# Optimization experiments

Hardware: AMD Instinct MI355X
Metric: run time of the kernel (lower is better)

Reference implementation:

```python
import jax, jax.numpy as jnp
import numpy as np

IN_DIM = 2048


def setup_inputs() -> dict:
    key = jax.random.key(0)
    ks = jax.random.split(key, 7)
    s = 1.0 / np.sqrt(IN_DIM)
    x = jax.random.normal(ks[0], (8, 256, IN_DIM), dtype=jnp.float32)
    Wq = jax.random.uniform(ks[1], (IN_DIM, IN_DIM), jnp.float32, -s, s)
    bq = jax.random.uniform(ks[2], (IN_DIM,), jnp.float32, -s, s)
    Wk = jax.random.uniform(ks[3], (IN_DIM, IN_DIM), jnp.float32, -s, s)
    bk = jax.random.uniform(ks[4], (IN_DIM,), jnp.float32, -s, s)
    Wv = jax.random.uniform(ks[5], (IN_DIM, IN_DIM), jnp.float32, -s, s)
    bv = jax.random.uniform(ks[6], (IN_DIM,), jnp.float32, -s, s)
    return {"x": x, "Wq": Wq, "bq": bq, "Wk": Wk, "bk": bk, "Wv": Wv, "bv": bv}


def reference(x, Wq, bq, Wk, bk, Wv, bv):
    # x: [B, C, L]; Linear acts on last (L) axis; torch Linear: y = x @ W^T + b
    scale = 1.0 / jnp.sqrt(jnp.asarray(x.shape[-1], x.dtype))
    q = jnp.einsum('bcl,ml->bcm', x, Wq) + bq
    k = jnp.einsum('bcl,ml->bcm', x, Wk) + bk
    v = jnp.einsum('bcl,ml->bcm', x, Wv) + bv
    # attn[b,l,m] = sum_c q[b,c,l] * k[b,c,m]
    attn = jnp.einsum('bcl,bcm->blm', q, k) * scale  # [B, L, L]
    attn = jax.nn.softmax(attn, axis=-1)
    # out[b,c,l] = sum_m v[b,c,m] * attn[b,l,m]
    out = jnp.einsum('bcm,blm->bcl', v, attn)  # [B, C, L]
    return out
```

## Files before the change

### kernel.cpp

```cpp
#include <hip/hip_runtime.h>
#include <hip/hip_bf16.h>
#include <cstdint>
#include <cstddef>


typedef __bf16 bf16_t;
typedef _Float16 fp16_t;
typedef __bf16 bf16x8 __attribute__((ext_vector_type(8)));
typedef __bf16 bf16x4 __attribute__((ext_vector_type(4)));
typedef float floatx4 __attribute__((ext_vector_type(4)));

#define GLD_LDS16(gptr, lptr)                                                  \
  __builtin_amdgcn_global_load_lds(                                            \
      (const __attribute__((address_space(1))) void*)(gptr),                   \
      (__attribute__((address_space(3))) void*)(lptr), 16, 0, 0)

#define BARRAW()                                                               \
  do {                                                                         \
    __builtin_amdgcn_sched_barrier(0);                                         \
    asm volatile("" ::: "memory");                                             \
    __builtin_amdgcn_s_barrier();                                              \
    __builtin_amdgcn_sched_barrier(0);                                         \
  } while (0)

__global__ __launch_bounds__(256) void cvt4_f32_bf16(
    const float* __restrict__ s0, const float* __restrict__ s1,
    const float* __restrict__ s2, const float* __restrict__ s3,
    bf16_t* __restrict__ d0, bf16_t* __restrict__ d1,
    bf16_t* __restrict__ d2, bf16_t* __restrict__ d3) {
  const float* s;
  bf16_t* d;
  switch (blockIdx.y) {
    case 0: s = s0; d = d0; break;
    case 1: s = s1; d = d1; break;
    case 2: s = s2; d = d2; break;
    default: s = s3; d = d3; break;
  }
  const int i = (blockIdx.x * 256 + threadIdx.x) * 4;
  const float4 v = *reinterpret_cast<const float4*>(s + i);
  bf16x4 o;
  o[0] = (bf16_t)v.x; o[1] = (bf16_t)v.y; o[2] = (bf16_t)v.z; o[3] = (bf16_t)v.w;
  *reinterpret_cast<bf16x4*>(d + i) = o;
}

__global__ __launch_bounds__(512, 2) void gemm_qkv8(
    const bf16_t* __restrict__ xb, const bf16_t* __restrict__ Wp,
    bf16_t* __restrict__ tT, bf16_t* __restrict__ vb,
    const float* __restrict__ bq, const float* __restrict__ bk,
    const float* __restrict__ bv) {
  __shared__ __align__(16) bf16_t As[2 * 16384];
  __shared__ __align__(16) bf16_t Bs[2 * 16384];

  constexpr long M4 = 4l * 1024 * 1024;
  const int tid = threadIdx.x, lane = tid & 63, w = tid >> 6;
  const int i15 = lane & 15, g4 = lane >> 4;
  const int wm = w >> 2, wn = w & 3;

  const int o = blockIdx.x;
  const int swz = (o & 7) * 24 + (o >> 3);
  const int mx = swz & 7, nx = swz >> 3;
  const int brow = mx * 256, bcol = nx * 256;

  const int srow = tid >> 2, sslot = tid & 3;
  const bf16_t* Ag = xb + (size_t)(brow + srow) * 2048 + sslot * 8;
  const bf16_t* Bg = Wp + (size_t)(bcol + srow) * 2048 + sslot * 8;

  auto stage_ht = [&](int h) {
    const int tile = h >> 2, buf = tile & 1, part = h & 3;
    const int kk = part >> 1;
    const bool isA = part & 1;
    const bf16_t* g = (isA ? Ag : Bg) + tile * 64 + kk * 32;
    bf16_t* l = (isA ? As : Bs) + buf * 16384 + kk * 8192 + w * 512;
    GLD_LDS16(g, l);
    GLD_LDS16(g + (size_t)128 * 2048, l + 4096);
  };

  floatx4 acc[8][4];
#pragma unroll
  for (int m = 0; m < 8; m++)
#pragma unroll
    for (int n = 0; n < 4; n++) acc[m][n] = (floatx4)0.f;

  bf16x8 Ar[4], Br[4];

#define LDA(buf, kk, mh)                                                       \
  {                                                                            \
    const bf16_t* ab = As + (buf) * 16384 + (kk) * 8192 +                      \
                       (wm * 128 + (mh) * 64 + i15) * 32 + g4 * 8;             \
    Ar[0] = *(const bf16x8*)&ab[0 * 512];                                      \
    Ar[1] = *(const bf16x8*)&ab[1 * 512];                                      \
    Ar[2] = *(const bf16x8*)&ab[2 * 512];                                      \
    Ar[3] = *(const bf16x8*)&ab[3 * 512];                                      \
  }
#define LDB(buf, kk)                                                           \
  {                                                                            \
    const bf16_t* bb = Bs + (buf) * 16384 + (kk) * 8192 +                      \
                       (wn * 64 + i15) * 32 + g4 * 8;                          \
    Br[0] = *(const bf16x8*)&bb[0 * 512];                                      \
    Br[1] = *(const bf16x8*)&bb[1 * 512];                                      \
    Br[2] = *(const bf16x8*)&bb[2 * 512];                                      \
    Br[3] = *(const bf16x8*)&bb[3 * 512];                                      \
  }
#define MMA(mh)                                                                \
  {                                                                            \
    __builtin_amdgcn_s_setprio(1);                                             \
    _Pragma("unroll") for (int mf = 0; mf < 4; mf++)                           \
        _Pragma("unroll") for (int nf = 0; nf < 4; nf++)                       \
        acc[(mh) * 4 + mf][nf] = __builtin_amdgcn_mfma_f32_16x16x32_bf16(      \
            Ar[mf], Br[nf], acc[(mh) * 4 + mf][nf], 0, 0, 0);                  \
    __builtin_amdgcn_s_setprio(0);                                             \
  }

  for (int h = 0; h < 7; ++h) stage_ht(h);
  asm volatile("s_waitcnt vmcnt(6)" ::: "memory");
  BARRAW();

  for (int j = 0; j < 16; ++j) {
    const int hb = 8 * j + 6;
    LDB(0, 0); LDA(0, 0, 0);
    stage_ht(hb + 1); BARRAW(); MMA(0); BARRAW();
    LDA(0, 0, 1);
    if (hb + 2 < 128) stage_ht(hb + 2); BARRAW(); MMA(1); BARRAW();
    LDB(0, 1); LDA(0, 1, 0);
    if (hb + 3 < 128) stage_ht(hb + 3); BARRAW(); MMA(0);
    BARRAW();
    LDA(0, 1, 1);
    if (hb + 4 < 128) stage_ht(hb + 4); BARRAW(); MMA(1);
    __builtin_amdgcn_sched_barrier(0);
    if (j == 15)
      asm volatile("s_waitcnt vmcnt(0)" ::: "memory");
    else
      asm volatile("s_waitcnt vmcnt(6)" ::: "memory");
    BARRAW();
    LDB(1, 0); LDA(1, 0, 0);
    if (hb + 5 < 128) stage_ht(hb + 5); BARRAW(); MMA(0); BARRAW();
    LDA(1, 0, 1);
    if (hb + 6 < 128) stage_ht(hb + 6); BARRAW(); MMA(1); BARRAW();
    LDB(1, 1); LDA(1, 1, 0);
    if (hb + 7 < 128) stage_ht(hb + 7); BARRAW(); MMA(0); BARRAW();
    LDA(1, 1, 1);
    if (hb + 8 < 128) stage_ht(hb + 8); BARRAW(); MMA(1);
    __builtin_amdgcn_sched_barrier(0);
    if (j < 15) asm volatile("s_waitcnt vmcnt(6)" ::: "memory");
    BARRAW();
  }
#undef LDA
#undef LDB
#undef MMA

#pragma unroll
  for (int nf = 0; nf < 4; nf++) {
    const int gj = bcol + wn * 64 + nf * 16 + i15;
    const int z = gj >> 11, jj = gj & 2047;
    const float* bp = (z == 0) ? bq : (z == 1) ? bk : bv;
    const float badd = bp[jj];
#pragma unroll
    for (int mf = 0; mf < 8; mf++) {
      const int gi = brow + wm * 128 + mf * 16 + g4 * 4;
      if (z < 2) {
        bf16x4 ov;
#pragma unroll
        for (int r = 0; r < 4; r++) ov[r] = (bf16_t)(acc[mf][nf][r] + badd);
        *(bf16x4*)&tT[(size_t)z * M4 + (size_t)jj * 2048 + gi] = ov;
      } else {
#pragma unroll
        for (int r = 0; r < 4; r++)
          vb[(size_t)(gi + r) * 2048 + jj] = (bf16_t)(acc[mf][nf][r] + badd);
      }
    }
  }
}

__global__ __launch_bounds__(256, 2) void flash3(
    const bf16_t* __restrict__ qT, const bf16_t* __restrict__ kT,
    const bf16_t* __restrict__ v, fp16_t* __restrict__ po,
    float* __restrict__ pl) {
  __shared__ __align__(16) bf16_t Ks[8192];
  __shared__ __align__(16) bf16_t Vs[8192];
  __shared__ __align__(16) bf16_t Ps[4 * 1280];

  const int tid = threadIdx.x, lane = tid & 63, w = tid >> 6;
  const int idx = blockIdx.x;
  const int b = idx & 7, sg = (idx >> 3) & 3, qt = idx >> 5;
  const int l0 = qt * 128;
  const int key0 = sg * 512;
  const int i15 = lane & 15, g4 = lane >> 4;

  const bf16_t* Qg = qT + (size_t)(l0 + w * 32) * 2048 + b * 256;
  const bf16_t* Kg = kT + (size_t)key0 * 2048 + b * 256;
  const bf16_t* Vg = v + (size_t)b * 256 * 2048 + key0;

  bf16x8 af0[8], af1[8];
#pragma unroll
  for (int ks = 0; ks < 8; ks++) {
    af0[ks] = *(const bf16x8*)&Qg[(size_t)i15 * 2048 + ks * 32 + g4 * 8];
    af1[ks] = *(const bf16x8*)&Qg[(size_t)(16 + i15) * 2048 + ks * 32 + g4 * 8];
  }

  const int srow = lane >> 2;
  const int sslot = (lane & 3) ^ ((lane >> 3) & 3);
  auto stageK = [&](const bf16_t* g) {
#pragma unroll
    for (int j = 0; j < 4; j++) {
      const int ch = w * 4 + j, ks = ch >> 1, mseg = ch & 1;
      GLD_LDS16(g + (size_t)(mseg * 16 + srow) * 2048 + ks * 32 + sslot * 8,
                Ks + ch * 512);
    }
  };
  auto stageV = [&](const bf16_t* g) {
#pragma unroll
    for (int j = 0; j < 4; j++) {
      const int ch = w * 4 + j;
      GLD_LDS16(g + (size_t)(ch * 16 + srow) * 2048 + sslot * 8, Vs + ch * 512);
    }
  };

  floatx4 acc_o0[16], acc_o1[16];
#pragma unroll
  for (int cf = 0; cf < 16; cf++) {
    acc_o0[cf] = (floatx4)0.f;
    acc_o1[cf] = (floatx4)0.f;
  }
  floatx4 acc_l0 = (floatx4)0.f, acc_l1 = (floatx4)0.f;

  bf16x8 vones;
#pragma unroll
  for (int j = 0; j < 8; j++) vones[j] = (bf16_t)1.0f;

  const float SC = 0.031880107f;
  const int slotr = g4 ^ ((i15 >> 1) & 3);

  stageK(Kg);
  stageV(Vg);
  __syncthreads();

  for (int t = 0; t < 16; t++) {
    floatx4 s00 = (floatx4)0.f, s01 = (floatx4)0.f;
    floatx4 s10 = (floatx4)0.f, s11 = (floatx4)0.f;
#pragma unroll
    for (int ks = 0; ks < 8; ks++) {
      const bf16x8 b0 = *(const bf16x8*)&Ks[ks * 1024 + i15 * 32 + slotr * 8];
      const bf16x8 b1 =
          *(const bf16x8*)&Ks[ks * 1024 + (16 + i15) * 32 + slotr * 8];
      s00 = __builtin_amdgcn_mfma_f32_16x16x32_bf16(af0[ks], b0, s00, 0, 0, 0);
      s01 = __builtin_amdgcn_mfma_f32_16x16x32_bf16(af0[ks], b1, s01, 0, 0, 0);
      s10 = __builtin_amdgcn_mfma_f32_16x16x32_bf16(af1[ks], b0, s10, 0, 0, 0);
      s11 = __builtin_amdgcn_mfma_f32_16x16x32_bf16(af1[ks], b1, s11, 0, 0, 0);
    }
    __syncthreads();
    if (t < 15) stageK(Kg + (size_t)(t + 1) * 32 * 2048);

    bf16_t* Pw = Ps + w * 1280;
#pragma unroll
    for (int r = 0; r < 4; r++) {
      Pw[(g4 * 4 + r) * 40 + i15] = (bf16_t)exp2f(s00[r] * SC);
      Pw[(g4 * 4 + r) * 40 + 16 + i15] = (bf16_t)exp2f(s01[r] * SC);
      Pw[(16 + g4 * 4 + r) * 40 + i15] = (bf16_t)exp2f(s10[r] * SC);
      Pw[(16 + g4 * 4 + r) * 40 + 16 + i15] = (bf16_t)exp2f(s11[r] * SC);
    }
    const bf16x8 pa0 = *(const bf16x8*)&Pw[i15 * 40 + g4 * 8];
    const bf16x8 pa1 = *(const bf16x8*)&Pw[(16 + i15) * 40 + g4 * 8];
    acc_l0 = __builtin_amdgcn_mfma_f32_16x16x32_bf16(pa0, vones, acc_l0, 0, 0, 0);
    acc_l1 = __builtin_amdgcn_mfma_f32_16x16x32_bf16(pa1, vones, acc_l1, 0, 0, 0);
#pragma unroll
    for (int cf = 0; cf < 16; cf++) {
      const bf16x8 bv = *(const bf16x8*)&Vs[(cf * 16 + i15) * 32 + slotr * 8];
      acc_o0[cf] = __builtin_amdgcn_mfma_f32_16x16x32_bf16(pa0, bv, acc_o0[cf], 0, 0, 0);
      acc_o1[cf] = __builtin_amdgcn_mfma_f32_16x16x32_bf16(pa1, bv, acc_o1[cf], 0, 0, 0);
    }
    __syncthreads();
    if (t < 15) stageV(Vg + (t + 1) * 32);
  }

  fp16_t* pob = po + ((size_t)(b * 4 + sg) * 2048 + l0 + w * 32) * 256;
#pragma unroll
  for (int cf = 0; cf < 16; cf++)
#pragma unroll
    for (int r = 0; r < 4; r++) {
      pob[(size_t)(g4 * 4 + r) * 256 + cf * 16 + i15] = (fp16_t)acc_o0[cf][r];
      pob[(size_t)(16 + g4 * 4 + r) * 256 + cf * 16 + i15] =
          (fp16_t)acc_o1[cf][r];
    }
  if (i15 == 0) {
    float* plb = pl + (size_t)(b * 4 + sg) * 2048 + l0 + w * 32;
#pragma unroll
    for (int r = 0; r < 4; r++) {
      plb[g4 * 4 + r] = acc_l0[r];
      plb[16 + g4 * 4 + r] = acc_l1[r];
    }
  }
}

__global__ __launch_bounds__(256) void combine4(
    const fp16_t* __restrict__ po, const float* __restrict__ pl,
    float* __restrict__ out) {
  __shared__ float invd[32];
  __shared__ float tile[32][33];
  const int lt = blockIdx.x, ct = blockIdx.y, b = blockIdx.z;
  const int l0 = lt * 32, c0 = ct * 32;
  const int t = threadIdx.x;

  if (t < 32) {
    float d = 0.f;
#pragma unroll
    for (int s = 0; s < 4; s++) d += pl[(size_t)(b * 4 + s) * 2048 + l0 + t];
    invd[t] = 1.f / d;
  }
  __syncthreads();

  const int c = t & 31;
#pragma unroll
  for (int pass = 0; pass < 4; pass++) {
    const int l = pass * 8 + (t >> 5);
    float acc = 0.f;
#pragma unroll
    for (int s = 0; s < 4; s++)
      acc += (float)po[((size_t)(b * 4 + s) * 2048 + l0 + l) * 256 + c0 + c];
    tile[c][l] = acc * invd[l];
  }
  __syncthreads();

  const int oc = t >> 3, lw = (t & 7) * 4;
  float4 val = {tile[oc][lw], tile[oc][lw + 1], tile[oc][lw + 2], tile[oc][lw + 3]};
  *(float4*)&out[((size_t)b * 256 + c0 + oc) * 2048 + l0 + lw] = val;
}

extern "C" void kernel_launch(void* const* d_in, const int* in_sizes, int n_in,
                              void* d_out, int out_size, void* d_ws,
                              size_t ws_size, hipStream_t stream) {
  const float* x = (const float*)d_in[0];
  float* out = (float*)d_out;

  constexpr long M4 = 4l * 1024 * 1024;
  bf16_t* ws = (bf16_t*)d_ws;
  bf16_t* xb = ws;
  bf16_t* Wb = ws + M4;
  bf16_t* tT = ws + 4 * M4;
  bf16_t* vb = ws + 6 * M4;
  fp16_t* po = (fp16_t*)(ws + 7 * M4);
  float* pl = (float*)(po + 8l * 4 * 2048 * 256);

  cvt4_f32_bf16<<<dim3(4096, 4), 256, 0, stream>>>(
      x, (const float*)d_in[1], (const float*)d_in[3], (const float*)d_in[5],
      xb, Wb, Wb + M4, Wb + 2 * M4);

  gemm_qkv8<<<dim3(192), 512, 0, stream>>>(
      xb, Wb, tT, vb, (const float*)d_in[2], (const float*)d_in[4],
      (const float*)d_in[6]);

  flash3<<<dim3(512), 256, 0, stream>>>(tT, tT + M4, vb, po, pl);

  combine4<<<dim3(64, 8, 8), 256, 0, stream>>>(po, pl, out);
}
```

Before: 234.1 us.

## Use XOR-swizzled 64-wide LDS tile layout and restage QKV GEMM pipeline

Changes the LDS layout of the QKV projection GEMM from two 32-column k-halves to a single 64-column row with an XOR swizzle on 16-byte chunks, and matches the global-to-LDS staging addresses and the fragment loads to it. The staging schedule is reorganised around per-matrix half-tile stages, with explicit lgkmcnt waits after the barriers and a peeled final iteration. The aim is to cut LDS bank conflicts on the fragment reads and simplify the prefetch bookkeeping. The extra lgkmcnt waits and the changed vmcnt depth may shift how well loads overlap with the MFMAs.

```diff
diff --git a/kernel.cpp b/kernel.cpp
--- a/kernel.cpp
+++ b/kernel.cpp
@@ -15,7 +15,17 @@
       (const __attribute__((address_space(1))) void*)(gptr),                   \
       (__attribute__((address_space(3))) void*)(lptr), 16, 0, 0)
 
-#define BARRAW()                                                               \
+#define SYNC_LGKM()                                                            \
+  do {                                                                         \
+    __builtin_amdgcn_sched_barrier(0);                                         \
+    asm volatile("" ::: "memory");                                             \
+    __builtin_amdgcn_s_barrier();                                              \
+    __builtin_amdgcn_sched_barrier(0);                                         \
+    asm volatile("s_waitcnt lgkmcnt(0)" ::: "memory");                         \
+    __builtin_amdgcn_sched_barrier(0);                                         \
+  } while (0)
+
+#define ENDB()                                                                 \
   do {                                                                         \
     __builtin_amdgcn_sched_barrier(0);                                         \
     asm volatile("" ::: "memory");                                             \
@@ -61,18 +71,20 @@
   const int mx = swz & 7, nx = swz >> 3;
   const int brow = mx * 256, bcol = nx * 256;
 
-  const int srow = tid >> 2, sslot = tid & 3;
-  const bf16_t* Ag = xb + (size_t)(brow + srow) * 2048 + sslot * 8;
-  const bf16_t* Bg = Wp + (size_t)(bcol + srow) * 2048 + sslot * 8;
-
-  auto stage_ht = [&](int h) {
-    const int tile = h >> 2, buf = tile & 1, part = h & 3;
-    const int kk = part >> 1;
-    const bool isA = part & 1;
-    const bf16_t* g = (isA ? Ag : Bg) + tile * 64 + kk * 32;
-    bf16_t* l = (isA ? As : Bs) + buf * 16384 + kk * 8192 + w * 512;
-    GLD_LDS16(g, l);
-    GLD_LDS16(g + (size_t)128 * 2048, l + 4096);
+  const int srow8 = tid >> 3;
+  const int sL = (tid & 7) ^ (srow8 & 7);
+  const bf16_t* Ag = xb + (size_t)(brow + srow8) * 2048 + sL * 8;
+  const bf16_t* Bg = Wp + (size_t)(bcol + srow8) * 2048 + sL * 8;
+
+  auto stageH = [&](int mat, int t, int half) {
+    const int buf = t & 1;
+#pragma unroll
+    for (int q = 0; q < 2; q++) {
+      const int c = half * 2 + q;
+      const bf16_t* g = (mat ? Ag : Bg) + (size_t)(c * 64) * 2048 + t * 64;
+      bf16_t* l = (mat ? As : Bs) + buf * 16384 + c * 4096 + w * 512;
+      GLD_LDS16(g, l);
+    }
   };
 
   floatx4 acc[8][4];
@@ -82,24 +94,26 @@
     for (int n = 0; n < 4; n++) acc[m][n] = (floatx4)0.f;
 
   bf16x8 Ar[4], Br[4];
-
+  const int ps0 = ((g4) ^ (i15 & 7)) * 8;
+  const int ps1 = ((4 + g4) ^ (i15 & 7)) * 8;
+
+#define LDB(buf, kk)                                                           \
+  {                                                                            \
+    const bf16_t* bb = Bs + (buf) * 16384 + (wn * 64 + i15) * 64 +             \
+                       ((kk) ? ps1 : ps0);                                     \
+    Br[0] = *(const bf16x8*)&bb[0];                                            \
+    Br[1] = *(const bf16x8*)&bb[1024];                                         \
+    Br[2] = *(const bf16x8*)&bb[2048];                                         \
+    Br[3] = *(const bf16x8*)&bb[3072];                                         \
+  }
 #define LDA(buf, kk, mh)                                                       \
   {                                                                            \
-    const bf16_t* ab = As + (buf) * 16384 + (kk) * 8192 +                      \
-                       (wm * 128 + (mh) * 64 + i15) * 32 + g4 * 8;             \
-    Ar[0] = *(const bf16x8*)&ab[0 * 512];                                      \
-    Ar[1] = *(const bf16x8*)&ab[1 * 512];                                      \
-    Ar[2] = *(const bf16x8*)&ab[2 * 512];                                      \
-    Ar[3] = *(const bf16x8*)&ab[3 * 512];                                      \
-  }
-#define LDB(buf, kk)                                                           \
-  {                                                                            \
-    const bf16_t* bb = Bs + (buf) * 16384 + (kk) * 8192 +                      \
-                       (wn * 64 + i15) * 32 + g4 * 8;                          \
-    Br[0] = *(const bf16x8*)&bb[0 * 512];                                      \
-    Br[1] = *(const bf16x8*)&bb[1 * 512];                                      \
-    Br[2] = *(const bf16x8*)&bb[2 * 512];                                      \
-    Br[3] = *(const bf16x8*)&bb[3 * 512];                                      \
+    const bf16_t* ab = As + (buf) * 16384 +                                    \
+                       (wm * 128 + (mh) * 64 + i15) * 64 + ((kk) ? ps1 : ps0); \
+    Ar[0] = *(const bf16x8*)&ab[0];                                            \
+    Ar[1] = *(const bf16x8*)&ab[1024];                                         \
+    Ar[2] = *(const bf16x8*)&ab[2048];                                         \
+    Ar[3] = *(const bf16x8*)&ab[3072];                                         \
   }
 #define MMA(mh)                                                                \
   {                                                                            \
@@ -111,39 +125,39 @@
     __builtin_amdgcn_s_setprio(0);                                             \
   }
 
-  for (int h = 0; h < 7; ++h) stage_ht(h);
-  asm volatile("s_waitcnt vmcnt(6)" ::: "memory");
-  BARRAW();
-
-  for (int j = 0; j < 16; ++j) {
-    const int hb = 8 * j + 6;
-    LDB(0, 0); LDA(0, 0, 0);
-    stage_ht(hb + 1); BARRAW(); MMA(0); BARRAW();
-    LDA(0, 0, 1);
-    if (hb + 2 < 128) stage_ht(hb + 2); BARRAW(); MMA(1); BARRAW();
-    LDB(0, 1); LDA(0, 1, 0);
-    if (hb + 3 < 128) stage_ht(hb + 3); BARRAW(); MMA(0);
-    BARRAW();
-    LDA(0, 1, 1);
-    if (hb + 4 < 128) stage_ht(hb + 4); BARRAW(); MMA(1);
+  stageH(1, 0, 0); stageH(0, 0, 0); stageH(1, 0, 1); stageH(0, 0, 1);
+  stageH(1, 1, 0);
+  asm volatile("s_waitcnt vmcnt(2)" ::: "memory");
+  ENDB();
+
+  for (int j = 0; j < 15; j++) {
+    const int t1 = 2 * j + 1, t2 = 2 * j + 2, t3 = 2 * j + 3;
+    LDB(0, 0); LDA(0, 0, 0); stageH(0, t1, 0); SYNC_LGKM(); MMA(0); ENDB();
+    LDA(0, 0, 1); stageH(1, t1, 1); SYNC_LGKM(); MMA(1); ENDB();
+    LDB(0, 1); LDA(0, 1, 0); stageH(0, t1, 1); SYNC_LGKM(); MMA(0); ENDB();
+    LDA(0, 1, 1); stageH(1, t2, 0); SYNC_LGKM(); MMA(1);
     __builtin_amdgcn_sched_barrier(0);
-    if (j == 15)
-      asm volatile("s_waitcnt vmcnt(0)" ::: "memory");
-    else
-      asm volatile("s_waitcnt vmcnt(6)" ::: "memory");
-    BARRAW();
-    LDB(1, 0); LDA(1, 0, 0);
-    if (hb + 5 < 128) stage_ht(hb + 5); BARRAW(); MMA(0); BARRAW();
-    LDA(1, 0, 1);
-    if (hb + 6 < 128) stage_ht(hb + 6); BARRAW(); MMA(1); BARRAW();
-    LDB(1, 1); LDA(1, 1, 0);
-    if (hb + 7 < 128) stage_ht(hb + 7); BARRAW(); MMA(0); BARRAW();
-    LDA(1, 1, 1);
-    if (hb + 8 < 128) stage_ht(hb + 8); BARRAW(); MMA(1);
+    asm volatile("s_waitcnt vmcnt(2)" ::: "memory");
+    ENDB();
+    LDB(1, 0); LDA(1, 0, 0); stageH(0, t2, 0); SYNC_LGKM(); MMA(0); ENDB();
+    LDA(1, 0, 1); stageH(1, t2, 1); SYNC_LGKM(); MMA(1); ENDB();
+    LDB(1, 1); LDA(1, 1, 0); stageH(0, t2, 1); SYNC_LGKM(); MMA(0); ENDB();
+    LDA(1, 1, 1); stageH(1, t3, 0); SYNC_LGKM(); MMA(1);
     __builtin_amdgcn_sched_barrier(0);
-    if (j < 15) asm volatile("s_waitcnt vmcnt(6)" ::: "memory");
-    BARRAW();
-  }
+    asm volatile("s_waitcnt vmcnt(2)" ::: "memory");
+    ENDB();
+  }
+  LDB(0, 0); LDA(0, 0, 0); stageH(0, 31, 0); SYNC_LGKM(); MMA(0); ENDB();
+  LDA(0, 0, 1); stageH(1, 31, 1); SYNC_LGKM(); MMA(1); ENDB();
+  LDB(0, 1); LDA(0, 1, 0); stageH(0, 31, 1); SYNC_LGKM(); MMA(0); ENDB();
+  LDA(0, 1, 1); SYNC_LGKM(); MMA(1);
+  __builtin_amdgcn_sched_barrier(0);
+  asm volatile("s_waitcnt vmcnt(0)" ::: "memory");
+  ENDB();
+  LDB(1, 0); LDA(1, 0, 0); SYNC_LGKM(); MMA(0); ENDB();
+  LDA(1, 0, 1); SYNC_LGKM(); MMA(1); ENDB();
+  LDB(1, 1); LDA(1, 1, 0); SYNC_LGKM(); MMA(0); ENDB();
+  LDA(1, 1, 1); SYNC_LGKM(); MMA(1);
 #undef LDA
 #undef LDB
 #undef MMA
```

New measurement: 234.9 us. About the same (+0.4%).

## Swizzle LDS layout and restructure QKV GEMM pipeline with shallower prefetch

Applied to the files above, without the earlier changes.

Adds an XOR swizzle of the 16-byte slot within each 32-element LDS row, applied on both the global-to-LDS staging and the fragment reads, to reduce LDS bank conflicts. Replaces the half-tile staging schedule, which kept seven stages in flight, with a per-tile macro that stages one quarter-tile per MMA phase using vmcnt(4) waits. Barriers no longer carry sched_barrier fences, which gives the compiler more freedom to schedule. The shallower prefetch and looser barriers risk exposing global load latency or ordering hazards.

```diff
diff --git a/kernel.cpp b/kernel.cpp
--- a/kernel.cpp
+++ b/kernel.cpp
@@ -15,13 +15,10 @@
       (const __attribute__((address_space(1))) void*)(gptr),                   \
       (__attribute__((address_space(3))) void*)(lptr), 16, 0, 0)
 
-#define BARRAW()                                                               \
-  do {                                                                         \
-    __builtin_amdgcn_sched_barrier(0);                                         \
-    asm volatile("" ::: "memory");                                             \
-    __builtin_amdgcn_s_barrier();                                              \
-    __builtin_amdgcn_sched_barrier(0);                                         \
-  } while (0)
+#define VM4 asm volatile("s_waitcnt vmcnt(4)" ::: "memory")
+#define VM0 asm volatile("s_waitcnt vmcnt(0)" ::: "memory")
+#define BAR1 asm volatile("s_barrier" ::: "memory")
+#define BAR2 __builtin_amdgcn_s_barrier()
 
 __global__ __launch_bounds__(256) void cvt4_f32_bf16(
     const float* __restrict__ s0, const float* __restrict__ s1,
@@ -48,8 +45,8 @@
     bf16_t* __restrict__ tT, bf16_t* __restrict__ vb,
     const float* __restrict__ bq, const float* __restrict__ bk,
     const float* __restrict__ bv) {
-  __shared__ __align__(16) bf16_t As[2 * 16384];
-  __shared__ __align__(16) bf16_t Bs[2 * 16384];
+  __shared__ __align__(16) bf16_t As[32768];
+  __shared__ __align__(16) bf16_t Bs[32768];
 
   constexpr long M4 = 4l * 1024 * 1024;
   const int tid = threadIdx.x, lane = tid & 63, w = tid >> 6;
@@ -61,18 +58,19 @@
   const int mx = swz & 7, nx = swz >> 3;
   const int brow = mx * 256, bcol = nx * 256;
 
-  const int srow = tid >> 2, sslot = tid & 3;
-  const bf16_t* Ag = xb + (size_t)(brow + srow) * 2048 + sslot * 8;
-  const bf16_t* Bg = Wp + (size_t)(bcol + srow) * 2048 + sslot * 8;
-
-  auto stage_ht = [&](int h) {
-    const int tile = h >> 2, buf = tile & 1, part = h & 3;
-    const int kk = part >> 1;
-    const bool isA = part & 1;
-    const bf16_t* g = (isA ? Ag : Bg) + tile * 64 + kk * 32;
-    bf16_t* l = (isA ? As : Bs) + buf * 16384 + kk * 8192 + w * 512;
-    GLD_LDS16(g, l);
-    GLD_LDS16(g + (size_t)128 * 2048, l + 4096);
+  const int srow = tid >> 2;
+  const int sL = (tid & 3) ^ ((tid >> 4) & 3);
+  const bf16_t* Ag = xb + (size_t)(brow + srow) * 2048 + sL * 8;
+  const bf16_t* Bg = Wp + (size_t)(bcol + srow) * 2048 + sL * 8;
+
+  auto stageH = [&](int mat, int t, int kk) {
+    const int buf = t & 1;
+#pragma unroll
+    for (int c = 0; c < 2; c++) {
+      const bf16_t* g = (mat ? Ag : Bg) + (size_t)(c * 128) * 2048 + t * 64 + kk * 32;
+      bf16_t* l = (mat ? As : Bs) + buf * 16384 + kk * 8192 + c * 4096 + w * 512;
+      GLD_LDS16(g, l);
+    }
   };
 
   floatx4 acc[8][4];
@@ -82,24 +80,25 @@
     for (int n = 0; n < 4; n++) acc[m][n] = (floatx4)0.f;
 
   bf16x8 Ar[4], Br[4];
-
+  const int ps = (g4 ^ ((i15 >> 2) & 3)) * 8;
+
+#define LDB(buf, kk)                                                           \
+  {                                                                            \
+    const bf16_t* bb =                                                         \
+        Bs + (buf) * 16384 + (kk) * 8192 + (wn * 64 + i15) * 32 + ps;          \
+    Br[0] = *(const bf16x8*)&bb[0];                                            \
+    Br[1] = *(const bf16x8*)&bb[512];                                          \
+    Br[2] = *(const bf16x8*)&bb[1024];                                         \
+    Br[3] = *(const bf16x8*)&bb[1536];                                         \
+  }
 #define LDA(buf, kk, mh)                                                       \
   {                                                                            \
     const bf16_t* ab = As + (buf) * 16384 + (kk) * 8192 +                      \
-                       (wm * 128 + (mh) * 64 + i15) * 32 + g4 * 8;             \
-    Ar[0] = *(const bf16x8*)&ab[0 * 512];                                      \
-    Ar[1] = *(const bf16x8*)&ab[1 * 512];                                      \
-    Ar[2] = *(const bf16x8*)&ab[2 * 512];                                      \
-    Ar[3] = *(const bf16x8*)&ab[3 * 512];                                      \
-  }
-#define LDB(buf, kk)                                                           \
-  {                                                                            \
-    const bf16_t* bb = Bs + (buf) * 16384 + (kk) * 8192 +                      \
-                       (wn * 64 + i15) * 32 + g4 * 8;                          \
-    Br[0] = *(const bf16x8*)&bb[0 * 512];                                      \
-    Br[1] = *(const bf16x8*)&bb[1 * 512];                                      \
-    Br[2] = *(const bf16x8*)&bb[2 * 512];                                      \
-    Br[3] = *(const bf16x8*)&bb[3 * 512];                                      \
+                       (wm * 128 + (mh) * 64 + i15) * 32 + ps;                 \
+    Ar[0] = *(const bf16x8*)&ab[0];                                            \
+    Ar[1] = *(const bf16x8*)&ab[512];                                          \
+    Ar[2] = *(const bf16x8*)&ab[1024];                                         \
+    Ar[3] = *(const bf16x8*)&ab[1536];                                         \
   }
 #define MMA(mh)                                                                \
   {                                                                            \
@@ -111,39 +110,25 @@
     __builtin_amdgcn_s_setprio(0);                                             \
   }
 
-  for (int h = 0; h < 7; ++h) stage_ht(h);
-  asm volatile("s_waitcnt vmcnt(6)" ::: "memory");
-  BARRAW();
-
-  for (int j = 0; j < 16; ++j) {
-    const int hb = 8 * j + 6;
-    LDB(0, 0); LDA(0, 0, 0);
-    stage_ht(hb + 1); BARRAW(); MMA(0); BARRAW();
-    LDA(0, 0, 1);
-    if (hb + 2 < 128) stage_ht(hb + 2); BARRAW(); MMA(1); BARRAW();
-    LDB(0, 1); LDA(0, 1, 0);
-    if (hb + 3 < 128) stage_ht(hb + 3); BARRAW(); MMA(0);
-    BARRAW();
-    LDA(0, 1, 1);
-    if (hb + 4 < 128) stage_ht(hb + 4); BARRAW(); MMA(1);
-    __builtin_amdgcn_sched_barrier(0);
-    if (j == 15)
-      asm volatile("s_waitcnt vmcnt(0)" ::: "memory");
-    else
-      asm volatile("s_waitcnt vmcnt(6)" ::: "memory");
-    BARRAW();
-    LDB(1, 0); LDA(1, 0, 0);
-    if (hb + 5 < 128) stage_ht(hb + 5); BARRAW(); MMA(0); BARRAW();
-    LDA(1, 0, 1);
-    if (hb + 6 < 128) stage_ht(hb + 6); BARRAW(); MMA(1); BARRAW();
-    LDB(1, 1); LDA(1, 1, 0);
-    if (hb + 7 < 128) stage_ht(hb + 7); BARRAW(); MMA(0); BARRAW();
-    LDA(1, 1, 1);
-    if (hb + 8 < 128) stage_ht(hb + 8); BARRAW(); MMA(1);
-    __builtin_amdgcn_sched_barrier(0);
-    if (j < 15) asm volatile("s_waitcnt vmcnt(6)" ::: "memory");
-    BARRAW();
-  }
+#define TILE_STG(buf, tn)                                                      \
+  LDB(buf, 0); LDA(buf, 0, 0); stageH(0, tn, 0); BAR1; MMA(0); BAR2;           \
+  LDA(buf, 0, 1); stageH(1, tn, 0); VM4; BAR1; MMA(1); BAR2;                   \
+  LDB(buf, 1); LDA(buf, 1, 0); stageH(0, tn, 1); BAR1; MMA(0); BAR2;           \
+  LDA(buf, 1, 1); stageH(1, tn, 1); VM4; BAR1; MMA(1); BAR2;
+
+  stageH(0, 0, 0); stageH(1, 0, 0); stageH(0, 0, 1); stageH(1, 0, 1);
+  VM4; BAR1;
+
+  for (int j = 0; j < 15; j++) {
+    TILE_STG(0, 2 * j + 1);
+    TILE_STG(1, 2 * j + 2);
+  }
+  TILE_STG(0, 31);
+  LDB(1, 0); LDA(1, 0, 0); BAR1; MMA(0); BAR2;
+  LDA(1, 0, 1); VM0; BAR1; MMA(1); BAR2;
+  LDB(1, 1); LDA(1, 1, 0); BAR1; MMA(0); BAR2;
+  LDA(1, 1, 1); MMA(1);
+#undef TILE_STG
 #undef LDA
 #undef LDB
 #undef MMA
```

After: 246.4 us. 5.3% more time.
